# Kernel optimization log

Hardware: AMD Instinct MI355X
Metric: run time of the kernel (lower is better)

## Reference

```python
import jax, jax.numpy as jnp
import numpy as np
import math

N_V, N_E, N_P = 50000, 10000, 800000
C_IN, C_HID, HEADS, N_CLS = 128, 64, 8, 40
SLOPE = 0.2   # atten_neg_slope
P_NORM = 1.0  # p for p_laplacian


def seg_softmax(s, seg, n):
    m = jax.ops.segment_max(s, seg, num_segments=n)
    ex = jnp.exp(s - m[seg])
    den = jax.ops.segment_sum(ex, seg, num_segments=n)
    return ex / (den[seg] + 1e-9)


def hgt_conv(X, W, b, a_v, a_e, v_ids, e_ids, n_e, is_last):
    """Hypergraph attention conv: vertex->edge->vertex with segment softmax attention."""
    n_v = X.shape[0]
    Xp = X @ W + b                                  # [N, C]
    xs = Xp[v_ids]                                  # [P, C] gather to incidence pairs
    al = seg_softmax(jax.nn.leaky_relu(xs @ a_v, SLOPE), e_ids, n_e)
    Ye = jax.ops.segment_sum(al[:, None] * xs, e_ids, num_segments=n_e)   # [E, C]
    ys = Ye[e_ids]                                  # [P, C]
    be = seg_softmax(jax.nn.leaky_relu(ys @ a_e, SLOPE), v_ids, n_v)
    Xo = jax.ops.segment_sum(be[:, None] * ys, v_ids, num_segments=n_v)   # [N, C]
    return Xo if is_last else jax.nn.relu(Xo)


def pos_encoding(X, C):
    n_v = X.shape[0]
    inv = 1.0 / C ** 0.5
    pos = jnp.arange(n_v, dtype=jnp.float32)[:, None]
    d1 = jnp.exp(jnp.arange(0, C, 2, dtype=jnp.float32) * (-math.log(10000.0) / C))
    d2 = jnp.exp(jnp.arange(1, C, 2, dtype=jnp.float32) * (-math.log(10000.0) / C))
    # interleave: even cols sin, odd cols cos
    pe = jnp.stack([jnp.sin(pos * d1), jnp.cos(pos * d2)], axis=-1).reshape(n_v, C) * inv
    p_lap = jnp.sum(jnp.abs(X) ** P_NORM, axis=1, keepdims=True) ** (1.0 / P_NORM)
    return p_lap * pe


def hspd_encoding(X, v_ids, e_ids, n_e):
    # degree-normalized two-hop (v->e->v) structural smoothing encoding
    n_v = X.shape[0]
    ones = jnp.ones(v_ids.shape[0], jnp.float32)
    de = jnp.maximum(jax.ops.segment_sum(ones, e_ids, num_segments=n_e), 1.0)
    dv = jnp.maximum(jax.ops.segment_sum(ones, v_ids, num_segments=n_v), 1.0)
    Xe = jax.ops.segment_sum(X[v_ids], e_ids, num_segments=n_e) / de[:, None]
    return jax.ops.segment_sum(Xe[e_ids], v_ids, num_segments=n_v) / dv[:, None]


def setup_inputs() -> dict:
    key = jax.random.key(0)
    ks = jax.random.split(key, 12)
    s = 0.02
    return {
        "X": jax.random.normal(ks[0], (N_V, C_IN), jnp.float32),
        "Wh": jax.random.normal(ks[1], (HEADS, C_IN, C_HID), jnp.float32) * s,
        "bh": jnp.zeros((HEADS, C_HID), jnp.float32),
        "avh": jax.random.normal(ks[2], (HEADS, C_HID), jnp.float32) * s,
        "aeh": jax.random.normal(ks[3], (HEADS, C_HID), jnp.float32) * s,
        "Wo": jax.random.normal(ks[4], (C_HID * HEADS, N_CLS), jnp.float32) * s,
        "bo": jnp.zeros((N_CLS,), jnp.float32),
        "avo": jax.random.normal(ks[5], (N_CLS,), jnp.float32) * s,
        "aeo": jax.random.normal(ks[6], (N_CLS,), jnp.float32) * s,
        "v_ids": jax.random.randint(ks[7], (N_P,), 0, N_V),
        "e_ids": jax.random.randint(ks[8], (N_P,), 0, N_E),
        "num_edges": N_E,
    }


def reference(X, Wh, bh, avh, aeh, Wo, bo, avo, aeo, v_ids, e_ids, num_edges):
    # multi-head HGTConv, concat over heads (dropout omitted: eval mode)
    heads = jax.vmap(lambda W, b, av, ae: hgt_conv(X, W, b, av, ae, v_ids, e_ids, num_edges, False))(Wh, bh, avh, aeh)           # [H, N, C_hid]
    Xt = jnp.moveaxis(heads, 0, 1).reshape(X.shape[0], -1)  # [N, H*C_hid]
    Xt = Xt + pos_encoding(Xt, Xt.shape[1])
    Xt = Xt + hspd_encoding(Xt, v_ids, e_ids, num_edges)
    return hgt_conv(Xt, Wo, bo, avo, aeo, v_ids, e_ids, num_edges, True)
```

## Files before the change

### kernel.cpp

```cpp
#include <hip/hip_runtime.h>
#include <math.h>

#define NV 50000
#define NE 10000
#define NP 800000
#define CH 512
#define NC 40
#define SLOPE 0.2f

__global__ __launch_bounds__(256) void k_hist(const int* __restrict__ v_ids, const int* __restrict__ e_ids,
                                              int* __restrict__ cnt_e, int* __restrict__ cnt_v)
{
  int i = blockIdx.x*256 + threadIdx.x;
  if(i<NP){ atomicAdd(&cnt_e[e_ids[i]],1); atomicAdd(&cnt_v[v_ids[i]],1); }
}

__global__ __launch_bounds__(1024) void k_scan(const int* __restrict__ cnt, int n,
                                               int* __restrict__ off, int* __restrict__ cur)
{
  __shared__ int wsum[16];
  __shared__ int runs;
  int tid=threadIdx.x, lane=tid&63, wid=tid>>6;
  if(tid==0) runs=0;
  __syncthreads();
  for(int base=0;base<n;base+=1024){
    int i=base+tid;
    int x=(i<n)?cnt[i]:0;
    int incl=x;
    #pragma unroll
    for(int d=1;d<64;d<<=1){ int v=__shfl_up(incl,d); if(lane>=d) incl+=v; }
    if(lane==63) wsum[wid]=incl;
    __syncthreads();
    int woff=0;
    for(int w=0;w<wid;w++) woff+=wsum[w];
    int excl=runs+woff+incl-x;
    if(i<n){ off[i]=excl; cur[i]=excl; }
    __syncthreads();
    if(tid==0){ int t=0; for(int w=0;w<16;w++) t+=wsum[w]; runs+=t; }
    __syncthreads();
  }
  if(tid==0) off[n]=runs;
}

__global__ __launch_bounds__(256) void k_scatter(const int* __restrict__ v_ids, const int* __restrict__ e_ids,
                                                 int* __restrict__ cur_e, int* __restrict__ cur_v,
                                                 int* __restrict__ gsrc_e, int* __restrict__ gsrc_v)
{
  int i = blockIdx.x*256+threadIdx.x;
  if(i<NP){
    int v = v_ids[i], e = e_ids[i];
    int pe = atomicAdd(&cur_e[e],1); gsrc_e[pe]=v;
    int pv = atomicAdd(&cur_v[v],1); gsrc_v[pv]=e;
  }
}

__global__ __launch_bounds__(256) void k_gemm1(const float* __restrict__ X, const float* __restrict__ Wh,
                                               const float* __restrict__ bh, float* __restrict__ Xp)
{
  __shared__ float As[32][64];
  __shared__ float Bs[32][64];
  int tid = threadIdx.x;
  int tx = tid & 15, ty = tid >> 4;
  int r0 = blockIdx.x * 64;
  int head = blockIdx.y;
  const float* Wb = Wh + (size_t)head*8192;
  float acc[4][4] = {};
  for(int k0=0;k0<128;k0+=32){
    #pragma unroll
    for(int rep=0;rep<2;rep++){
      int lin = rep*256 + tid;
      int row = lin >> 3;
      int q   = lin & 7;
      float4 v = make_float4(0.f,0.f,0.f,0.f);
      int gr = r0+row;
      if(gr < NV) v = *(const float4*)(X + (size_t)gr*128 + k0 + q*4);
      As[q*4+0][row]=v.x; As[q*4+1][row]=v.y; As[q*4+2][row]=v.z; As[q*4+3][row]=v.w;
    }
    #pragma unroll
    for(int rep=0;rep<2;rep++){
      int lin = rep*256 + tid;
      int kk = lin >> 4;
      int q  = lin & 15;
      *(float4*)&Bs[kk][q*4] = *(const float4*)(Wb + (size_t)(k0+kk)*64 + q*4);
    }
    __syncthreads();
    #pragma unroll
    for(int k=0;k<32;k++){
      float4 a = *(const float4*)&As[k][ty*4];
      float4 b = *(const float4*)&Bs[k][tx*4];
      acc[0][0]+=a.x*b.x; acc[0][1]+=a.x*b.y; acc[0][2]+=a.x*b.z; acc[0][3]+=a.x*b.w;
      acc[1][0]+=a.y*b.x; acc[1][1]+=a.y*b.y; acc[1][2]+=a.y*b.z; acc[1][3]+=a.y*b.w;
      acc[2][0]+=a.z*b.x; acc[2][1]+=a.z*b.y; acc[2][2]+=a.z*b.z; acc[2][3]+=a.z*b.w;
      acc[3][0]+=a.w*b.x; acc[3][1]+=a.w*b.y; acc[3][2]+=a.w*b.z; acc[3][3]+=a.w*b.w;
    }
    __syncthreads();
  }
  int n0 = head*64 + tx*4;
  float4 bias = *(const float4*)(bh + n0);
  #pragma unroll
  for(int i=0;i<4;i++){
    int gr = r0 + ty*4 + i;
    if(gr<NV){
      float4 o = make_float4(acc[i][0]+bias.x, acc[i][1]+bias.y, acc[i][2]+bias.z, acc[i][3]+bias.w);
      *(float4*)(Xp + (size_t)gr*CH + n0) = o;
    }
  }
}

__global__ __launch_bounds__(256) void k_rowscore8(const float* __restrict__ rows, int nr,
                                                   const float* __restrict__ avec,
                                                   float* __restrict__ rsc)
{
  int lane=threadIdx.x&63, wid=threadIdx.x>>6;
  int r = blockIdx.x*4+wid;
  if(r>=nr) return;
  const float* rr = rows + (size_t)r*CH + lane*8;
  float4 a0 = *(const float4*)(avec + lane*8);
  float4 a1 = *(const float4*)(avec + lane*8 + 4);
  float4 x0 = *(const float4*)rr;
  float4 x1 = *(const float4*)(rr+4);
  float s = x0.x*a0.x + x0.y*a0.y + x0.z*a0.z + x0.w*a0.w
          + x1.x*a1.x + x1.y*a1.y + x1.z*a1.z + x1.w*a1.w;
  s += __shfl_xor(s,1); s += __shfl_xor(s,2); s += __shfl_xor(s,4);
  s = (s>0.f) ? s : SLOPE*s;
  if((lane&7)==0) rsc[(size_t)r*8 + (lane>>3)] = s;
}

__global__ __launch_bounds__(256) void k_rowscore1(const float* __restrict__ rows, int nr,
                                                   const float* __restrict__ avec,
                                                   float* __restrict__ rsc)
{
  int lane=threadIdx.x&63, wid=threadIdx.x>>6;
  int r = blockIdx.x*4+wid;
  if(r>=nr) return;
  float x = (lane<NC)? rows[(size_t)r*NC+lane]*avec[lane] : 0.f;
  #pragma unroll
  for(int d=1;d<64;d<<=1) x += __shfl_xor(x,d);
  if(lane==0) rsc[r] = (x>0.f)? x : SLOPE*x;
}

template<bool RELU>
__global__ __launch_bounds__(256) void k_agg8(const float* __restrict__ rows,
                                              const int* __restrict__ gsrc,
                                              const int* __restrict__ off,
                                              const float* __restrict__ rsc,
                                              float* __restrict__ outm)
{
  __shared__ float red[4][CH];
  __shared__ float part[4][8];
  __shared__ float mh_s[8], dn_s[8];
  int e = blockIdx.x;
  int s0 = off[e], n = off[e+1]-s0;
  int tid=threadIdx.x, lane=tid&63, wid=tid>>6;
  int h8 = tid&7;
  float mloc = -INFINITY;
  for(int i=tid>>3; i<n; i+=32)
    mloc = fmaxf(mloc, rsc[(size_t)gsrc[s0+i]*8 + h8]);
  mloc = fmaxf(mloc, __shfl_xor(mloc,8));
  mloc = fmaxf(mloc, __shfl_xor(mloc,16));
  mloc = fmaxf(mloc, __shfl_xor(mloc,32));
  if(lane<8) part[wid][lane]=mloc;
  __syncthreads();
  if(tid<8) mh_s[tid] = fmaxf(fmaxf(part[0][tid],part[1][tid]), fmaxf(part[2][tid],part[3][tid]));
  __syncthreads();
  float mh8 = mh_s[h8];
  float dp = 0.f;
  for(int i=tid>>3; i<n; i+=32)
    dp += __expf(rsc[(size_t)gsrc[s0+i]*8 + h8] - mh8);
  dp += __shfl_xor(dp,8); dp += __shfl_xor(dp,16); dp += __shfl_xor(dp,32);
  if(lane<8) part[wid][lane]=dp;
  __syncthreads();
  if(tid<8) dn_s[tid] = part[0][tid]+part[1][tid]+part[2][tid]+part[3][tid];
  __syncthreads();
  int h = lane>>3;
  float mh = mh_s[h];
  float invd = 1.f/(dn_s[h]+1e-9f);
  float acc[8]={0,0,0,0,0,0,0,0};
  for(int i=wid;i<n;i+=4){
    int g = gsrc[s0+i];
    float al = __expf(rsc[(size_t)g*8+h] - mh) * invd;
    const float* r = rows + (size_t)g*CH + lane*8;
    float4 x0 = *(const float4*)r;
    float4 x1 = *(const float4*)(r+4);
    acc[0]+=al*x0.x; acc[1]+=al*x0.y; acc[2]+=al*x0.z; acc[3]+=al*x0.w;
    acc[4]+=al*x1.x; acc[5]+=al*x1.y; acc[6]+=al*x1.z; acc[7]+=al*x1.w;
  }
  #pragma unroll
  for(int j=0;j<8;j++) red[wid][lane*8+j]=acc[j];
  __syncthreads();
  for(int c=tid;c<CH;c+=256){
    float v = red[0][c]+red[1][c]+red[2][c]+red[3][c];
    if(RELU) v = v>0.f ? v : 0.f;
    outm[(size_t)e*CH+c] = v;
  }
}

__global__ void k_freq(float* __restrict__ freq){
  int c = blockIdx.x*256 + threadIdx.x;
  if(c<CH) freq[c] = (float)exp(-(double)c * 9.210340371976184 / 512.0);
}

__global__ __launch_bounds__(256) void k_pos(float* __restrict__ X, const float* __restrict__ freq)
{
  int lane=threadIdx.x&63, wid=threadIdx.x>>6;
  int v = blockIdx.x*4+wid;
  if(v>=NV) return;
  float* r = X + (size_t)v*CH + lane*8;
  float4 x0=*(float4*)r, x1=*(float4*)(r+4);
  float s = fabsf(x0.x)+fabsf(x0.y)+fabsf(x0.z)+fabsf(x0.w)
          + fabsf(x1.x)+fabsf(x1.y)+fabsf(x1.z)+fabsf(x1.w);
  #pragma unroll
  for(int d=1;d<64;d<<=1) s += __shfl_xor(s,d);
  const float inv = 0.04419417382415922f;
  float pos = (float)v;
  float xv[8] = {x0.x,x0.y,x0.z,x0.w,x1.x,x1.y,x1.z,x1.w};
  float o[8];
  #pragma unroll
  for(int j=0;j<8;j++){
    int c = lane*8+j;
    float ang = pos*freq[c];
    float pe = ((c&1)? cosf(ang) : sinf(ang))*inv;
    o[j] = xv[j] + s*pe;
  }
  float4 y0=make_float4(o[0],o[1],o[2],o[3]), y1=make_float4(o[4],o[5],o[6],o[7]);
  *(float4*)r = y0; *(float4*)(r+4)=y1;
}

__global__ __launch_bounds__(256) void k_avg8(const float* __restrict__ rows,
                                              const int* __restrict__ gsrc,
                                              const int* __restrict__ off,
                                              const int* __restrict__ cnt,
                                              const float* __restrict__ addbase,
                                              float* __restrict__ outm)
{
  __shared__ float red[4][CH];
  int e = blockIdx.x;
  int s0=off[e], n=off[e+1]-s0;
  int lane=threadIdx.x&63, wid=threadIdx.x>>6, tid=threadIdx.x;
  float acc[8]={0,0,0,0,0,0,0,0};
  for(int i=wid;i<n;i+=4){
    int g = gsrc[s0+i];
    const float* r = rows + (size_t)g*CH + lane*8;
    float4 x0=*(const float4*)r, x1=*(const float4*)(r+4);
    acc[0]+=x0.x; acc[1]+=x0.y; acc[2]+=x0.z; acc[3]+=x0.w;
    acc[4]+=x1.x; acc[5]+=x1.y; acc[6]+=x1.z; acc[7]+=x1.w;
  }
  #pragma unroll
  for(int j=0;j<8;j++) red[wid][lane*8+j]=acc[j];
  __syncthreads();
  int c0 = cnt[e];
  float scale = 1.f/(float)(c0>1?c0:1);
  for(int c=tid;c<CH;c+=256){
    float v=(red[0][c]+red[1][c]+red[2][c]+red[3][c])*scale;
    if(addbase) v += addbase[(size_t)e*CH+c];
    outm[(size_t)e*CH+c]=v;
  }
}

__global__ __launch_bounds__(256) void k_gemm2(const float* __restrict__ Xt, const float* __restrict__ Wo,
                                               const float* __restrict__ bo, float* __restrict__ Xp2)
{
  __shared__ float rs[16*516];
  int tid=threadIdx.x;
  int r0 = blockIdx.x*16;
  for(int lin=tid; lin<2048; lin+=256){
    int row = lin>>7; int q = lin&127;
    int gr = r0+row;
    float4 v=make_float4(0.f,0.f,0.f,0.f);
    if(gr<NV) v = *(const float4*)(Xt + (size_t)gr*CH + q*4);
    *(float4*)&rs[row*516+q*4] = v;
  }
  __syncthreads();
  for(int idx=tid; idx<16*NC; idx+=256){
    int r = idx/NC, n = idx%NC;
    int gr = r0+r;
    if(gr>=NV) continue;
    const float* rr = &rs[r*516];
    float acc=0.f;
    #pragma unroll 8
    for(int k=0;k<CH;k++) acc += rr[k]*Wo[(size_t)k*NC+n];
    Xp2[(size_t)gr*NC+n] = acc + bo[n];
  }
}

__global__ __launch_bounds__(256) void k_agg1(const float* __restrict__ rows,
                                              const int* __restrict__ gsrc,
                                              const int* __restrict__ off,
                                              const float* __restrict__ rsc,
                                              float* __restrict__ outm)
{
  __shared__ float red[4][NC];
  __shared__ float part[4];
  __shared__ float mh_sh, dn_sh;
  int e = blockIdx.x;
  int s0=off[e], n=off[e+1]-s0;
  int tid=threadIdx.x, lane=tid&63, wid=tid>>6;
  float mloc=-INFINITY;
  for(int i=tid;i<n;i+=256) mloc=fmaxf(mloc, rsc[gsrc[s0+i]]);
  #pragma unroll
  for(int d=1;d<64;d<<=1) mloc=fmaxf(mloc,__shfl_xor(mloc,d));
  if(lane==0) part[wid]=mloc;
  __syncthreads();
  if(tid==0) mh_sh = fmaxf(fmaxf(part[0],part[1]),fmaxf(part[2],part[3]));
  __syncthreads();
  float mh = mh_sh;
  float dp=0.f;
  for(int i=tid;i<n;i+=256) dp += __expf(rsc[gsrc[s0+i]] - mh);
  #pragma unroll
  for(int d=1;d<64;d<<=1) dp += __shfl_xor(dp,d);
  if(lane==0) part[wid]=dp;
  __syncthreads();
  if(tid==0) dn_sh = part[0]+part[1]+part[2]+part[3];
  __syncthreads();
  float invd = 1.f/(dn_sh+1e-9f);
  float acc=0.f;
  for(int i=wid;i<n;i+=4){
    int g = gsrc[s0+i];
    float al = __expf(rsc[g]-mh)*invd;
    float x = (lane<NC)? rows[(size_t)g*NC+lane] : 0.f;
    acc += al*x;
  }
  if(lane<NC) red[wid][lane]=acc;
  __syncthreads();
  if(tid<NC) outm[(size_t)e*NC+tid] = red[0][tid]+red[1][tid]+red[2][tid]+red[3][tid];
}

extern "C" void kernel_launch(void* const* d_in, const int* in_sizes, int n_in,
                              void* d_out, int out_size, void* d_ws, size_t ws_size,
                              hipStream_t stream)
{
  (void)in_sizes; (void)n_in; (void)out_size; (void)ws_size;
  const float* X   = (const float*)d_in[0];
  const float* Wh  = (const float*)d_in[1];
  const float* bh  = (const float*)d_in[2];
  const float* avh = (const float*)d_in[3];
  const float* aeh = (const float*)d_in[4];
  const float* Wo  = (const float*)d_in[5];
  const float* bo  = (const float*)d_in[6];
  const float* avo = (const float*)d_in[7];
  const float* aeo = (const float*)d_in[8];
  const int* v_ids = (const int*)d_in[9];
  const int* e_ids = (const int*)d_in[10];
  float* out = (float*)d_out;

  char* w = (char*)d_ws;
  auto alloc = [&](size_t bytes)->char*{ char* p=w; w += (bytes+255)&~(size_t)255; return p; };
  int* cnt_e  = (int*)alloc((size_t)NE*4);
  int* cnt_v  = (int*)alloc((size_t)NV*4);
  int* off_e  = (int*)alloc((size_t)(NE+1)*4);
  int* off_v  = (int*)alloc((size_t)(NV+1)*4);
  int* cur_e  = (int*)alloc((size_t)NE*4);
  int* cur_v  = (int*)alloc((size_t)NV*4);
  int* gsrc_e = (int*)alloc((size_t)NP*4);
  int* gsrc_v = (int*)alloc((size_t)NP*4);
  float* rsc_v = (float*)alloc((size_t)NV*8*4);
  float* rsc_e = (float*)alloc((size_t)NE*8*4);
  float* rs1_v = (float*)alloc((size_t)NV*4);
  float* rs1_e = (float*)alloc((size_t)NE*4);
  float* Xp   = (float*)alloc((size_t)NV*CH*4);
  float* Ye   = (float*)alloc((size_t)NE*CH*4);
  float* Xp2  = (float*)alloc((size_t)NV*NC*4);
  float* Ye2  = (float*)alloc((size_t)NE*NC*4);
  float* freq = (float*)alloc((size_t)CH*4);

  hipMemsetAsync(cnt_e, 0, (size_t)NE*4, stream);
  hipMemsetAsync(cnt_v, 0, (size_t)NV*4, stream);

  const int PB = (NP+255)/256;

  k_hist<<<PB,256,0,stream>>>(v_ids,e_ids,cnt_e,cnt_v);
  k_scan<<<1,1024,0,stream>>>(cnt_e,NE,off_e,cur_e);
  k_scan<<<1,1024,0,stream>>>(cnt_v,NV,off_v,cur_v);
  k_scatter<<<PB,256,0,stream>>>(v_ids,e_ids,cur_e,cur_v,gsrc_e,gsrc_v);

  k_gemm1<<<dim3((NV+63)/64, 8),256,0,stream>>>(X,Wh,bh,Xp);
  k_rowscore8<<<(NV+3)/4,256,0,stream>>>(Xp, NV, avh, rsc_v);
  k_agg8<false><<<NE,256,0,stream>>>(Xp, gsrc_e, off_e, rsc_v, Ye);
  k_rowscore8<<<(NE+3)/4,256,0,stream>>>(Ye, NE, aeh, rsc_e);
  k_agg8<true><<<NV,256,0,stream>>>(Ye, gsrc_v, off_v, rsc_e, Xp);

  k_freq<<<2,256,0,stream>>>(freq);
  k_pos<<<(NV+3)/4,256,0,stream>>>(Xp, freq);

  k_avg8<<<NE,256,0,stream>>>(Xp, gsrc_e, off_e, cnt_e, nullptr, Ye);
  k_avg8<<<NV,256,0,stream>>>(Ye, gsrc_v, off_v, cnt_v, Xp, Xp);

  k_gemm2<<<(NV+15)/16,256,0,stream>>>(Xp, Wo, bo, Xp2);
  k_rowscore1<<<(NV+3)/4,256,0,stream>>>(Xp2, NV, avo, rs1_v);
  k_agg1<<<NE,256,0,stream>>>(Xp2, gsrc_e, off_e, rs1_v, Ye2);
  k_rowscore1<<<(NE+3)/4,256,0,stream>>>(Ye2, NE, aeo, rs1_e);
  k_agg1<<<NV,256,0,stream>>>(Ye2, gsrc_v, off_v, rs1_e, out);
}
```

Before: 1.758 ms.

## Fuse attention scoring and positional encoding into GEMM and aggregation epilogues

Measured after the change: 1.693 ms. 1.04x faster.

```diff
diff --git a/kernel.cpp b/kernel.cpp
--- a/kernel.cpp
+++ b/kernel.cpp
@@ -7,6 +7,7 @@
 #define CH 512
 #define NC 40
 #define SLOPE 0.2f
+#define PINV 0.04419417382415922f
 
 __global__ __launch_bounds__(256) void k_hist(const int* __restrict__ v_ids, const int* __restrict__ e_ids,
                                               int* __restrict__ cnt_e, int* __restrict__ cnt_v)
@@ -23,18 +24,24 @@
   int tid=threadIdx.x, lane=tid&63, wid=tid>>6;
   if(tid==0) runs=0;
   __syncthreads();
-  for(int base=0;base<n;base+=1024){
-    int i=base+tid;
-    int x=(i<n)?cnt[i]:0;
-    int incl=x;
+  for(int base=0;base<n;base+=8192){
+    int i0 = base + tid*8;
+    int x[8]; int tsum=0;
+    #pragma unroll
+    for(int j=0;j<8;j++){ x[j] = (i0+j<n)?cnt[i0+j]:0; tsum+=x[j]; }
+    int incl=tsum;
     #pragma unroll
     for(int d=1;d<64;d<<=1){ int v=__shfl_up(incl,d); if(lane>=d) incl+=v; }
     if(lane==63) wsum[wid]=incl;
     __syncthreads();
     int woff=0;
     for(int w=0;w<wid;w++) woff+=wsum[w];
-    int excl=runs+woff+incl-x;
-    if(i<n){ off[i]=excl; cur[i]=excl; }
+    int run = runs + woff + incl - tsum;
+    #pragma unroll
+    for(int j=0;j<8;j++){
+      if(i0+j<n){ off[i0+j]=run; cur[i0+j]=run; }
+      run += x[j];
+    }
     __syncthreads();
     if(tid==0){ int t=0; for(int w=0;w<16;w++) t+=wsum[w]; runs+=t; }
     __syncthreads();
@@ -55,10 +62,12 @@
 }
 
 __global__ __launch_bounds__(256) void k_gemm1(const float* __restrict__ X, const float* __restrict__ Wh,
-                                               const float* __restrict__ bh, float* __restrict__ Xp)
+                                               const float* __restrict__ bh, const float* __restrict__ avh,
+                                               float* __restrict__ Xp, float* __restrict__ rsc_v)
 {
   __shared__ float As[32][64];
   __shared__ float Bs[32][64];
+  __shared__ float scp[64][17];
   int tid = threadIdx.x;
   int tx = tid & 15, ty = tid >> 4;
   int r0 = blockIdx.x * 64;
@@ -97,58 +106,42 @@
   }
   int n0 = head*64 + tx*4;
   float4 bias = *(const float4*)(bh + n0);
+  float4 av   = *(const float4*)(avh + n0);
   #pragma unroll
   for(int i=0;i<4;i++){
     int gr = r0 + ty*4 + i;
+    float4 o = make_float4(acc[i][0]+bias.x, acc[i][1]+bias.y, acc[i][2]+bias.z, acc[i][3]+bias.w);
+    if(gr<NV) *(float4*)(Xp + (size_t)gr*CH + n0) = o;
+    scp[ty*4+i][tx] = o.x*av.x + o.y*av.y + o.z*av.z + o.w*av.w;
+  }
+  __syncthreads();
+  if(tid<64){
+    int gr = r0 + tid;
     if(gr<NV){
-      float4 o = make_float4(acc[i][0]+bias.x, acc[i][1]+bias.y, acc[i][2]+bias.z, acc[i][3]+bias.w);
-      *(float4*)(Xp + (size_t)gr*CH + n0) = o;
-    }
-  }
-}
-
-__global__ __launch_bounds__(256) void k_rowscore8(const float* __restrict__ rows, int nr,
-                                                   const float* __restrict__ avec,
-                                                   float* __restrict__ rsc)
-{
-  int lane=threadIdx.x&63, wid=threadIdx.x>>6;
-  int r = blockIdx.x*4+wid;
-  if(r>=nr) return;
-  const float* rr = rows + (size_t)r*CH + lane*8;
-  float4 a0 = *(const float4*)(avec + lane*8);
-  float4 a1 = *(const float4*)(avec + lane*8 + 4);
-  float4 x0 = *(const float4*)rr;
-  float4 x1 = *(const float4*)(rr+4);
-  float s = x0.x*a0.x + x0.y*a0.y + x0.z*a0.z + x0.w*a0.w
-          + x1.x*a1.x + x1.y*a1.y + x1.z*a1.z + x1.w*a1.w;
-  s += __shfl_xor(s,1); s += __shfl_xor(s,2); s += __shfl_xor(s,4);
-  s = (s>0.f) ? s : SLOPE*s;
-  if((lane&7)==0) rsc[(size_t)r*8 + (lane>>3)] = s;
-}
-
-__global__ __launch_bounds__(256) void k_rowscore1(const float* __restrict__ rows, int nr,
-                                                   const float* __restrict__ avec,
-                                                   float* __restrict__ rsc)
-{
-  int lane=threadIdx.x&63, wid=threadIdx.x>>6;
-  int r = blockIdx.x*4+wid;
-  if(r>=nr) return;
-  float x = (lane<NC)? rows[(size_t)r*NC+lane]*avec[lane] : 0.f;
-  #pragma unroll
-  for(int d=1;d<64;d<<=1) x += __shfl_xor(x,d);
-  if(lane==0) rsc[r] = (x>0.f)? x : SLOPE*x;
-}
-
-template<bool RELU>
+      float s=0.f;
+      #pragma unroll
+      for(int t=0;t<16;t++) s += scp[tid][t];
+      s = (s>0.f)? s : SLOPE*s;
+      rsc_v[(size_t)gr*8 + head] = s;
+    }
+  }
+}
+
+template<int MODE>
 __global__ __launch_bounds__(256) void k_agg8(const float* __restrict__ rows,
                                               const int* __restrict__ gsrc,
                                               const int* __restrict__ off,
                                               const float* __restrict__ rsc,
-                                              float* __restrict__ outm)
+                                              float* __restrict__ outm,
+                                              const float* __restrict__ aevec,
+                                              float* __restrict__ rsc_out,
+                                              const float* __restrict__ freq)
 {
   __shared__ float red[4][CH];
   __shared__ float part[4][8];
   __shared__ float mh_s[8], dn_s[8];
+  __shared__ float sc[CH];
+  __shared__ float L1s;
   int e = blockIdx.x;
   int s0 = off[e], n = off[e+1]-s0;
   int tid=threadIdx.x, lane=tid&63, wid=tid>>6;
@@ -188,42 +181,49 @@
   #pragma unroll
   for(int j=0;j<8;j++) red[wid][lane*8+j]=acc[j];
   __syncthreads();
-  for(int c=tid;c<CH;c+=256){
-    float v = red[0][c]+red[1][c]+red[2][c]+red[3][c];
-    if(RELU) v = v>0.f ? v : 0.f;
-    outm[(size_t)e*CH+c] = v;
+  if(MODE==0){
+    for(int c=tid;c<CH;c+=256){
+      float v = red[0][c]+red[1][c]+red[2][c]+red[3][c];
+      outm[(size_t)e*CH+c] = v;
+      sc[c] = v*aevec[c];
+    }
+    __syncthreads();
+    if(tid<8){
+      float s=0.f;
+      #pragma unroll
+      for(int k=0;k<64;k++) s += sc[tid*64+k];
+      s = (s>0.f)? s : SLOPE*s;
+      rsc_out[(size_t)e*8+tid] = s;
+    }
+  } else {
+    int c0=tid, c1=tid+256;
+    float v0 = red[0][c0]+red[1][c0]+red[2][c0]+red[3][c0];
+    float v1 = red[0][c1]+red[1][c1]+red[2][c1]+red[3][c1];
+    v0 = v0>0.f? v0:0.f;
+    v1 = v1>0.f? v1:0.f;
+    sc[tid] = v0+v1;
+    __syncthreads();
+    if(tid<64){
+      float s = sc[tid]+sc[tid+64]+sc[tid+128]+sc[tid+192];
+      #pragma unroll
+      for(int d=1;d<64;d<<=1) s += __shfl_xor(s,d);
+      if(tid==0) L1s = s;
+    }
+    __syncthreads();
+    float L1 = L1s;
+    float pos = (float)e;
+    float a0 = pos*freq[c0];
+    float p0 = ((c0&1)? cosf(a0) : sinf(a0))*PINV;
+    float a1 = pos*freq[c1];
+    float p1 = ((c1&1)? cosf(a1) : sinf(a1))*PINV;
+    outm[(size_t)e*CH+c0] = v0 + L1*p0;
+    outm[(size_t)e*CH+c1] = v1 + L1*p1;
   }
 }
 
 __global__ void k_freq(float* __restrict__ freq){
   int c = blockIdx.x*256 + threadIdx.x;
   if(c<CH) freq[c] = (float)exp(-(double)c * 9.210340371976184 / 512.0);
-}
-
-__global__ __launch_bounds__(256) void k_pos(float* __restrict__ X, const float* __restrict__ freq)
-{
-  int lane=threadIdx.x&63, wid=threadIdx.x>>6;
-  int v = blockIdx.x*4+wid;
-  if(v>=NV) return;
-  float* r = X + (size_t)v*CH + lane*8;
-  float4 x0=*(float4*)r, x1=*(float4*)(r+4);
-  float s = fabsf(x0.x)+fabsf(x0.y)+fabsf(x0.z)+fabsf(x0.w)
-          + fabsf(x1.x)+fabsf(x1.y)+fabsf(x1.z)+fabsf(x1.w);
-  #pragma unroll
-  for(int d=1;d<64;d<<=1) s += __shfl_xor(s,d);
-  const float inv = 0.04419417382415922f;
-  float pos = (float)v;
-  float xv[8] = {x0.x,x0.y,x0.z,x0.w,x1.x,x1.y,x1.z,x1.w};
-  float o[8];
-  #pragma unroll
-  for(int j=0;j<8;j++){
-    int c = lane*8+j;
-    float ang = pos*freq[c];
-    float pe = ((c&1)? cosf(ang) : sinf(ang))*inv;
-    o[j] = xv[j] + s*pe;
-  }
-  float4 y0=make_float4(o[0],o[1],o[2],o[3]), y1=make_float4(o[4],o[5],o[6],o[7]);
-  *(float4*)r = y0; *(float4*)(r+4)=y1;
 }
 
 __global__ __launch_bounds__(256) void k_avg8(const float* __restrict__ rows,
@@ -258,9 +258,11 @@
 }
 
 __global__ __launch_bounds__(256) void k_gemm2(const float* __restrict__ Xt, const float* __restrict__ Wo,
-                                               const float* __restrict__ bo, float* __restrict__ Xp2)
+                                               const float* __restrict__ bo, const float* __restrict__ avo,
+                                               float* __restrict__ Xp2, float* __restrict__ rs1_v)
 {
   __shared__ float rs[16*516];
+  __shared__ float sc2[16][41];
   int tid=threadIdx.x;
   int r0 = blockIdx.x*16;
   for(int lin=tid; lin<2048; lin+=256){
@@ -279,19 +281,36 @@
     float acc=0.f;
     #pragma unroll 8
     for(int k=0;k<CH;k++) acc += rr[k]*Wo[(size_t)k*NC+n];
-    Xp2[(size_t)gr*NC+n] = acc + bo[n];
-  }
-}
-
+    float o = acc + bo[n];
+    Xp2[(size_t)gr*NC+n] = o;
+    sc2[r][n] = o*avo[n];
+  }
+  __syncthreads();
+  if(tid<16){
+    int gr = r0+tid;
+    if(gr<NV){
+      float s=0.f;
+      #pragma unroll
+      for(int k=0;k<NC;k++) s += sc2[tid][k];
+      s = (s>0.f)? s : SLOPE*s;
+      rs1_v[gr] = s;
+    }
+  }
+}
+
+template<bool SC>
 __global__ __launch_bounds__(256) void k_agg1(const float* __restrict__ rows,
                                               const int* __restrict__ gsrc,
                                               const int* __restrict__ off,
                                               const float* __restrict__ rsc,
-                                              float* __restrict__ outm)
+                                              float* __restrict__ outm,
+                                              const float* __restrict__ aevec,
+                                              float* __restrict__ rsout)
 {
   __shared__ float red[4][NC];
   __shared__ float part[4];
   __shared__ float mh_sh, dn_sh;
+  __shared__ float scb[NC];
   int e = blockIdx.x;
   int s0=off[e], n=off[e+1]-s0;
   int tid=threadIdx.x, lane=tid&63, wid=tid>>6;
@@ -322,7 +341,20 @@
   }
   if(lane<NC) red[wid][lane]=acc;
   __syncthreads();
-  if(tid<NC) outm[(size_t)e*NC+tid] = red[0][tid]+red[1][tid]+red[2][tid]+red[3][tid];
+  if(tid<NC){
+    float val = red[0][tid]+red[1][tid]+red[2][tid]+red[3][tid];
+    outm[(size_t)e*NC+tid] = val;
+    if(SC) scb[tid] = val*aevec[tid];
+  }
+  if(SC){
+    __syncthreads();
+    if(tid==0){
+      float s=0.f;
+      #pragma unroll
+      for(int k=0;k<NC;k++) s += scb[k];
+      rsout[e] = (s>0.f)? s : SLOPE*s;
+    }
+  }
 }
 
 extern "C" void kernel_launch(void* const* d_in, const int* in_sizes, int n_in,
@@ -363,6 +395,7 @@
   float* Ye2  = (float*)alloc((size_t)NE*NC*4);
   float* freq = (float*)alloc((size_t)CH*4);
 
+  k_freq<<<2,256,0,stream>>>(freq);
   hipMemsetAsync(cnt_e, 0, (size_t)NE*4, stream);
   hipMemsetAsync(cnt_v, 0, (size_t)NV*4, stream);
 
@@ -373,21 +406,14 @@
   k_scan<<<1,1024,0,stream>>>(cnt_v,NV,off_v,cur_v);
   k_scatter<<<PB,256,0,stream>>>(v_ids,e_ids,cur_e,cur_v,gsrc_e,gsrc_v);
 
-  k_gemm1<<<dim3((NV+63)/64, 8),256,0,stream>>>(X,Wh,bh,Xp);
-  k_rowscore8<<<(NV+3)/4,256,0,stream>>>(Xp, NV, avh, rsc_v);
-  k_agg8<false><<<NE,256,0,stream>>>(Xp, gsrc_e, off_e, rsc_v, Ye);
-  k_rowscore8<<<(NE+3)/4,256,0,stream>>>(Ye, NE, aeh, rsc_e);
-  k_agg8<true><<<NV,256,0,stream>>>(Ye, gsrc_v, off_v, rsc_e, Xp);
-
-  k_freq<<<2,256,0,stream>>>(freq);
-  k_pos<<<(NV+3)/4,256,0,stream>>>(Xp, freq);
+  k_gemm1<<<dim3((NV+63)/64, 8),256,0,stream>>>(X,Wh,bh,avh,Xp,rsc_v);
+  k_agg8<0><<<NE,256,0,stream>>>(Xp, gsrc_e, off_e, rsc_v, Ye, aeh, rsc_e, nullptr);
+  k_agg8<1><<<NV,256,0,stream>>>(Ye, gsrc_v, off_v, rsc_e, Xp, nullptr, nullptr, freq);
 
   k_avg8<<<NE,256,0,stream>>>(Xp, gsrc_e, off_e, cnt_e, nullptr, Ye);
   k_avg8<<<NV,256,0,stream>>>(Ye, gsrc_v, off_v, cnt_v, Xp, Xp);
 
-  k_gemm2<<<(NV+15)/16,256,0,stream>>>(Xp, Wo, bo, Xp2);
-  k_rowscore1<<<(NV+3)/4,256,0,stream>>>(Xp2, NV, avo, rs1_v);
-  k_agg1<<<NE,256,0,stream>>>(Xp2, gsrc_e, off_e, rs1_v, Ye2);
-  k_rowscore1<<<(NE+3)/4,256,0,stream>>>(Ye2, NE, aeo, rs1_e);
-  k_agg1<<<NV,256,0,stream>>>(Ye2, gsrc_v, off_v, rs1_e, out);
-}
+  k_gemm2<<<(NV+15)/16,256,0,stream>>>(Xp, Wo, bo, avo, Xp2, rs1_v);
+  k_agg1<true><<<NE,256,0,stream>>>(Xp2, gsrc_e, off_e, rs1_v, Ye2, aeo, rs1_e);
+  k_agg1<false><<<NV,256,0,stream>>>(Ye2, gsrc_v, off_v, rs1_e, out, nullptr, nullptr);
+}
```
